# Performance work log

Hardware: AMD Instinct MI355X
Metric: run time of the kernel (lower is better)

The kernel has to match this reference:

```python
import jax, jax.numpy as jnp
import numpy as np

SIZE = 100
NUM_PARAMS = 5
DEPTH = 10            # complete binary tree: 2**DEPTH - 1 = 1023 nodes, 512 leaves
NUM_TREES = 1024
NUM_NODES = 2 ** DEPTH - 1


def setup_inputs() -> dict:
    key = jax.random.key(0)
    ks = jax.random.split(key, 7)
    times = jax.random.uniform(ks[0], (NUM_TREES, NUM_NODES), dtype=jnp.float32) + 0.1
    # Linear(1, size): weight column vector + bias
    Qw = jax.random.normal(ks[1], (SIZE,), dtype=jnp.float32) * 0.5
    Qb = jax.random.normal(ks[2], (SIZE,), dtype=jnp.float32) * 0.1
    # Linear(size, size): scaled so deep relu chain stays stable
    Ww = jax.random.normal(ks[3], (SIZE, SIZE), dtype=jnp.float32) * (0.5 / np.sqrt(SIZE))
    Wb = jax.random.normal(ks[4], (SIZE,), dtype=jnp.float32) * 0.1
    # Linear(size, num_params)
    Pw = jax.random.normal(ks[5], (NUM_PARAMS, SIZE), dtype=jnp.float32) * (1.0 / np.sqrt(SIZE))
    Pb = jax.random.normal(ks[6], (NUM_PARAMS,), dtype=jnp.float32) * 0.1
    return {"times": times, "Qw": Qw, "Qb": Qb, "Ww": Ww, "Wb": Wb, "Pw": Pw, "Pb": Pb}


def reference(times, Qw, Qb, Ww, Wb, Pw, Pb):
    """Batched, level-synchronous version of gRNN.traverse over complete binary trees.

    times: [B, 2**D - 1] node times in heap order (node i -> children 2i+1, 2i+2).
    Leaf:     h = relu(Q(t))
    Internal: h = relu(W(h_left + h_right) + Q(t))
    Root output projected to num_params. Same math as the recursive torch code.
    """
    B, N = times.shape
    D = int(np.log2(N + 1))
    # leaf level (deepest): Q(t) = t * Qw + Qb  (Linear(1, size))
    s = 2 ** (D - 1) - 1
    h = jax.nn.relu(times[:, s:s + 2 ** (D - 1), None] * Qw + Qb)  # [B, 2^(D-1), size]
    for d in range(D - 2, -1, -1):  # fixed small loop over tree depth
        s = 2 ** d - 1
        t = times[:, s:s + 2 ** d, None]                 # [B, 2^d, 1]
        comb = h[:, 0::2] + h[:, 1::2]                   # left + right children
        h = jax.nn.relu(jnp.einsum('bns,os->bno', comb, Ww) + Wb + t * Qw + Qb)
    root = h[:, 0]                                       # [B, size]
    return root @ Pw.T + Pb                              # [B, num_params]
```

## Files before the change

### kernel.cpp

```cpp
#include <hip/hip_runtime.h>

typedef _Float16 h8 __attribute__((ext_vector_type(8)));
typedef _Float16 h4 __attribute__((ext_vector_type(4)));
typedef float f4 __attribute__((ext_vector_type(4)));
typedef unsigned int uint32;

#define NT 7
#define KC 4
#define HSTRIDE 108

__global__ __launch_bounds__(256, 2)
void grnn_fused(const float* __restrict__ times,
                const float* __restrict__ Qw,
                const float* __restrict__ Qb,
                const float* __restrict__ Ww,
                const float* __restrict__ Wb,
                const float* __restrict__ Pw,
                const float* __restrict__ Pb,
                float* __restrict__ out)
{
  __shared__ __align__(16) _Float16 Hs[256][HSTRIDE];
  __shared__ __align__(8)  _Float16 ts[1026];
  __shared__ __align__(16) float qw_s[128];
  __shared__ __align__(16) float qb_s[128];

  const int tid  = threadIdx.x;
  const int wave = tid >> 6;
  const int lane = tid & 63;
  const int l15  = lane & 15;
  const int kg   = lane >> 4;
  const int tree = blockIdx.x;

  {
    const float* tg = times + tree * 1023;
    for (int i = tid; i < 1023; i += 256) ts[1 + i] = (_Float16)tg[i];
    if (tid == 0) ts[0] = (_Float16)0.f;
    if (tid < 128) {
      float qw = 0.f, qb = 0.f;
      if (tid < 100) { qw = Qw[tid]; qb = Qb[tid]; }
      qw_s[tid] = qw; qb_s[tid] = qb;
    }
  }

  h8 wf[NT][KC];
  #pragma unroll
  for (int nt = 0; nt < NT; ++nt) {
    const int r = nt * 16 + l15;
    #pragma unroll
    for (int kc = 0; kc < KC; ++kc) {
      h8 v;
      #pragma unroll
      for (int j = 0; j < 8; ++j) v[j] = (_Float16)0.f;
      if (r < 100) {
        const int kb = kc * 32 + kg * 8;
        if (kc < 3) {
          const f4 w0 = *(const f4*)&Ww[r * 100 + kb];
          const f4 w1 = *(const f4*)&Ww[r * 100 + kb + 4];
          #pragma unroll
          for (int j = 0; j < 4; ++j) {
            v[j]     = (_Float16)w0[j];
            v[j + 4] = (_Float16)w1[j];
          }
        } else if (kg == 0) {
          const f4 w0 = *(const f4*)&Ww[r * 100 + 96];
          #pragma unroll
          for (int j = 0; j < 4; ++j) v[j] = (_Float16)w0[j];
          v[4] = (_Float16)Qw[r];
          v[5] = (_Float16)(Qb[r] + Wb[r]);
        }
      }
      wf[nt][kc] = v;
    }
  }
  __syncthreads();

#define DO_MT(MT) do {                                                        \
    _Pragma("unroll")                                                         \
    for (int nt_ = 0; nt_ < NT; ++nt_) {                                      \
      f4 acc_ = {0.f, 0.f, 0.f, 0.f};                                         \
      _Pragma("unroll")                                                       \
      for (int kc_ = 0; kc_ < KC; ++kc_)                                      \
        acc_ = __builtin_amdgcn_mfma_f32_16x16x32_f16(af[kc_], wf[nt_][kc_],  \
                                                      acc_, 0, 0, 0);         \
      const int o_ = nt_ * 16 + l15;                                          \
      if (o_ < 100) {                                                         \
        const int mr_ = (MT) * 16 + kg * 4;                                   \
        _Pragma("unroll")                                                     \
        for (int r_ = 0; r_ < 4; ++r_)                                        \
          Hs[mr_ + r_][o_] = (_Float16)fmaxf(acc_[r_], 0.f);                  \
      }                                                                       \
    }                                                                         \
  } while (0)

#define LOAD_AFR(MT, S) do {                                                  \
    const int m2_ = ((MT) * 16 + l15) * 2;                                    \
    _Pragma("unroll")                                                         \
    for (int kc_ = 0; kc_ < 3; ++kc_) {                                       \
      const int kb_ = kc_ * 32 + kg * 8;                                      \
      h4 a0_ = *(const h4*)&Hs[m2_][kb_];                                     \
      h4 b0_ = *(const h4*)&Hs[m2_][kb_ + 4];                                 \
      h4 a1_ = *(const h4*)&Hs[m2_ + 1][kb_];                                 \
      h4 b1_ = *(const h4*)&Hs[m2_ + 1][kb_ + 4];                             \
      h4 lo_ = a0_ + a1_, hi_ = b0_ + b1_;                                    \
      af[kc_] = __builtin_shufflevector(lo_, hi_, 0, 1, 2, 3, 4, 5, 6, 7);    \
    }                                                                         \
    if (kg == 0) {                                                            \
      h4 a0_ = *(const h4*)&Hs[m2_][96];                                      \
      h4 a1_ = *(const h4*)&Hs[m2_ + 1][96];                                  \
      h4 lo_ = a0_ + a1_;                                                     \
      h4 hi_ = {ts[1 + (S) + (MT) * 16 + l15], (_Float16)1.f,                 \
                (_Float16)0.f, (_Float16)0.f};                                \
      af[3] = __builtin_shufflevector(lo_, hi_, 0, 1, 2, 3, 4, 5, 6, 7);      \
    } else {                                                                  \
      _Pragma("unroll")                                                       \
      for (int j_ = 0; j_ < 8; ++j_) af[3][j_] = (_Float16)0.f;               \
    }                                                                         \
  } while (0)

  #pragma unroll 1
  for (int i = 0; i < 4; ++i) {
    const int mt = wave + 4 * i;
    const int m  = mt * 16 + l15;
    const uint32 tp = *(const uint32*)&ts[512 + 2 * m];
    const float t0 = (float)*(const _Float16*)&tp;
    const float t1 = (float)*((const _Float16*)&tp + 1);
    h8 af[KC];
    #pragma unroll
    for (int kc = 0; kc < KC; ++kc) {
      const int kb = kc * 32 + kg * 8;
      const f4 qwa = *(const f4*)&qw_s[kb];
      const f4 qwb = *(const f4*)&qw_s[kb + 4];
      const f4 qba = *(const f4*)&qb_s[kb];
      const f4 qbb = *(const f4*)&qb_s[kb + 4];
      #pragma unroll
      for (int j = 0; j < 4; ++j) {
        float h0 = fmaxf(t0 * qwa[j] + qba[j], 0.f);
        float h1 = fmaxf(t1 * qwa[j] + qba[j], 0.f);
        af[kc][j] = (_Float16)(h0 + h1);
        float g0 = fmaxf(t0 * qwb[j] + qbb[j], 0.f);
        float g1 = fmaxf(t1 * qwb[j] + qbb[j], 0.f);
        af[kc][j + 4] = (_Float16)(g0 + g1);
      }
    }
    if (kg == 0) {
      af[3][4] = ts[1 + 255 + m];
      af[3][5] = (_Float16)1.f;
      af[3][6] = (_Float16)0.f;
      af[3][7] = (_Float16)0.f;
    }
    DO_MT(mt);
  }

  #pragma unroll 1
  for (int d = 7; d >= 0; --d) {
    const int s  = (1 << d) - 1;
    const int nm = (d >= 4) ? (1 << (d - 4)) : 1;
    const bool mine = wave < (nm < 4 ? nm : 4);
    h8 af[KC];
    if (mine) LOAD_AFR(wave, s);
    __syncthreads();
    if (mine) {
      DO_MT(wave);
      if (nm == 8) {
        LOAD_AFR(wave + 4, s);
        DO_MT(wave + 4);
      }
    }
    __syncthreads();
  }

  if (tid < 160) {
    const int p = tid >> 5;
    const int j = tid & 31;
    float sum = 0.f;
    #pragma unroll
    for (int c = 0; c < 4; ++c) {
      const int o = j + 32 * c;
      if (o < 100) sum += (float)Hs[0][o] * Pw[p * 100 + o];
    }
    sum += __shfl_down(sum, 16, 32);
    sum += __shfl_down(sum, 8, 32);
    sum += __shfl_down(sum, 4, 32);
    sum += __shfl_down(sum, 2, 32);
    sum += __shfl_down(sum, 1, 32);
    if (j == 0) out[tree * 5 + p] = sum + Pb[p];
  }
#undef DO_MT
#undef LOAD_AFR
}

extern "C" void kernel_launch(void* const* d_in, const int* in_sizes, int n_in,
                              void* d_out, int out_size, void* d_ws, size_t ws_size,
                              hipStream_t stream) {
  (void)n_in; (void)out_size; (void)d_ws; (void)ws_size;
  const float* times = (const float*)d_in[0];
  const float* Qw = (const float*)d_in[1];
  const float* Qb = (const float*)d_in[2];
  const float* Ww = (const float*)d_in[3];
  const float* Wb = (const float*)d_in[4];
  const float* Pw = (const float*)d_in[5];
  const float* Pb = (const float*)d_in[6];
  float* outp = (float*)d_out;
  const int B = in_sizes[0] / 1023;
  grnn_fused<<<dim3(B), dim3(256), 0, stream>>>(times, Qw, Qb, Ww, Wb, Pw, Pb, outp);
}
```

Measured before the change: 105.3 us.

## Pre-sum sibling children in registers, double-buffer LDS, and split upper levels across waves

The MFMA operands are swapped so each lane holds outputs of adjacent nodes. Sibling outputs are then summed with a lane shuffle before being written to LDS as combined child rows. LDS is double-buffered (read/write halves alternate per level), which drops one __syncthreads per level, and loads become single h8 reads with no adds. For the small upper levels the output tiles are split across all four waves instead of leaving three idle. This adds shuffles and more complex indexing, and risks correctness in the buffer indexing.

New measurement: 106.6 us. No clear change (+1.3%).

```diff
diff --git a/kernel.cpp b/kernel.cpp
--- a/kernel.cpp
+++ b/kernel.cpp
@@ -7,7 +7,7 @@
 
 #define NT 7
 #define KC 4
-#define HSTRIDE 108
+#define HSTRIDE 104
 
 __global__ __launch_bounds__(256, 2)
 void grnn_fused(const float* __restrict__ times,
@@ -19,7 +19,7 @@
                 const float* __restrict__ Pb,
                 float* __restrict__ out)
 {
-  __shared__ __align__(16) _Float16 Hs[256][HSTRIDE];
+  __shared__ __align__(16) _Float16 Cs[192][HSTRIDE];
   __shared__ __align__(8)  _Float16 ts[1026];
   __shared__ __align__(16) float qw_s[128];
   __shared__ __align__(16) float qb_s[128];
@@ -74,40 +74,58 @@
   }
   __syncthreads();
 
-#define DO_MT(MT) do {                                                        \
+#define DO_MT(MT, LO, HI, WB) do {                                            \
     _Pragma("unroll")                                                         \
     for (int nt_ = 0; nt_ < NT; ++nt_) {                                      \
-      f4 acc_ = {0.f, 0.f, 0.f, 0.f};                                         \
-      _Pragma("unroll")                                                       \
-      for (int kc_ = 0; kc_ < KC; ++kc_)                                      \
-        acc_ = __builtin_amdgcn_mfma_f32_16x16x32_f16(af[kc_], wf[nt_][kc_],  \
-                                                      acc_, 0, 0, 0);         \
-      const int o_ = nt_ * 16 + l15;                                          \
-      if (o_ < 100) {                                                         \
-        const int mr_ = (MT) * 16 + kg * 4;                                   \
+      if (nt_ >= (LO) && nt_ < (HI)) {                                        \
+        f4 acc_ = {0.f, 0.f, 0.f, 0.f};                                       \
         _Pragma("unroll")                                                     \
-        for (int r_ = 0; r_ < 4; ++r_)                                        \
-          Hs[mr_ + r_][o_] = (_Float16)fmaxf(acc_[r_], 0.f);                  \
+        for (int kc_ = 0; kc_ < KC; ++kc_)                                    \
+          acc_ = __builtin_amdgcn_mfma_f32_16x16x32_f16(wf[nt_][kc_],         \
+                                                        af[kc_], acc_, 0,0,0);\
+        if (nt_ < 6 || kg == 0) {                                             \
+          h4 hv_ = {(_Float16)fmaxf(acc_[0], 0.f),                            \
+                    (_Float16)fmaxf(acc_[1], 0.f),                            \
+                    (_Float16)fmaxf(acc_[2], 0.f),                            \
+                    (_Float16)fmaxf(acc_[3], 0.f)};                           \
+          uint2 u_ = __builtin_bit_cast(uint2, hv_);                          \
+          u_.x = __shfl_xor(u_.x, 1, 64);                                     \
+          u_.y = __shfl_xor(u_.y, 1, 64);                                     \
+          hv_ = hv_ + __builtin_bit_cast(h4, u_);                             \
+          if ((l15 & 1) == 0)                                                 \
+            *(h4*)&Cs[(WB) + (MT) * 8 + (l15 >> 1)][nt_ * 16 + kg * 4] = hv_; \
+        }                                                                     \
       }                                                                       \
     }                                                                         \
   } while (0)
 
-#define LOAD_AFR(MT, S) do {                                                  \
-    const int m2_ = ((MT) * 16 + l15) * 2;                                    \
+#define DO_MT_ROOT(LO, HI) do {                                               \
     _Pragma("unroll")                                                         \
-    for (int kc_ = 0; kc_ < 3; ++kc_) {                                       \
-      const int kb_ = kc_ * 32 + kg * 8;                                      \
-      h4 a0_ = *(const h4*)&Hs[m2_][kb_];                                     \
-      h4 b0_ = *(const h4*)&Hs[m2_][kb_ + 4];                                 \
-      h4 a1_ = *(const h4*)&Hs[m2_ + 1][kb_];                                 \
-      h4 b1_ = *(const h4*)&Hs[m2_ + 1][kb_ + 4];                             \
-      h4 lo_ = a0_ + a1_, hi_ = b0_ + b1_;                                    \
-      af[kc_] = __builtin_shufflevector(lo_, hi_, 0, 1, 2, 3, 4, 5, 6, 7);    \
+    for (int nt_ = 0; nt_ < NT; ++nt_) {                                      \
+      if (nt_ >= (LO) && nt_ < (HI)) {                                        \
+        f4 acc_ = {0.f, 0.f, 0.f, 0.f};                                       \
+        _Pragma("unroll")                                                     \
+        for (int kc_ = 0; kc_ < KC; ++kc_)                                    \
+          acc_ = __builtin_amdgcn_mfma_f32_16x16x32_f16(wf[nt_][kc_],         \
+                                                        af[kc_], acc_, 0,0,0);\
+        if ((nt_ < 6 || kg == 0) && l15 == 0) {                               \
+          h4 hv_ = {(_Float16)fmaxf(acc_[0], 0.f),                            \
+                    (_Float16)fmaxf(acc_[1], 0.f),                            \
+                    (_Float16)fmaxf(acc_[2], 0.f),                            \
+                    (_Float16)fmaxf(acc_[3], 0.f)};                           \
+          *(h4*)&Cs[0][nt_ * 16 + kg * 4] = hv_;                              \
+        }                                                                     \
+      }                                                                       \
     }                                                                         \
+  } while (0)
+
+#define LOAD_AFR(MT, S, RB) do {                                              \
+    const int row_ = (RB) + (MT) * 16 + l15;                                  \
+    _Pragma("unroll")                                                         \
+    for (int kc_ = 0; kc_ < 3; ++kc_)                                         \
+      af[kc_] = *(const h8*)&Cs[row_][kc_ * 32 + kg * 8];                     \
     if (kg == 0) {                                                            \
-      h4 a0_ = *(const h4*)&Hs[m2_][96];                                      \
-      h4 a1_ = *(const h4*)&Hs[m2_ + 1][96];                                  \
-      h4 lo_ = a0_ + a1_;                                                     \
+      h4 lo_ = *(const h4*)&Cs[row_][96];                                     \
       h4 hi_ = {ts[1 + (S) + (MT) * 16 + l15], (_Float16)1.f,                 \
                 (_Float16)0.f, (_Float16)0.f};                                \
       af[3] = __builtin_shufflevector(lo_, hi_, 0, 1, 2, 3, 4, 5, 6, 7);      \
@@ -148,26 +166,47 @@
       af[3][6] = (_Float16)0.f;
       af[3][7] = (_Float16)0.f;
     }
-    DO_MT(mt);
-  }
+    DO_MT(mt, 0, NT, 0);
+  }
+  __syncthreads();
 
   #pragma unroll 1
-  for (int d = 7; d >= 0; --d) {
+  for (int d = 7; d >= 1; --d) {
     const int s  = (1 << d) - 1;
+    const int R  = ((7 - d) & 1) ? 128 : 0;
+    const int W  = 128 - R;
     const int nm = (d >= 4) ? (1 << (d - 4)) : 1;
-    const bool mine = wave < (nm < 4 ? nm : 4);
     h8 af[KC];
-    if (mine) LOAD_AFR(wave, s);
+    if (nm >= 4) {
+      LOAD_AFR(wave, s, R);
+      DO_MT(wave, 0, NT, W);
+      if (nm == 8) {
+        LOAD_AFR(wave + 4, s, R);
+        DO_MT(wave + 4, 0, NT, W);
+      }
+    } else if (nm == 2) {
+      const int mt = wave & 1;
+      const int lo = (wave < 2) ? 0 : 4;
+      const int hi = (wave < 2) ? 4 : NT;
+      LOAD_AFR(mt, s, R);
+      DO_MT(mt, lo, hi, W);
+    } else {
+      const int lo = 2 * wave;
+      const int hi = (wave == 3) ? NT : 2 * wave + 2;
+      LOAD_AFR(0, s, R);
+      DO_MT(0, lo, hi, W);
+    }
     __syncthreads();
-    if (mine) {
-      DO_MT(wave);
-      if (nm == 8) {
-        LOAD_AFR(wave + 4, s);
-        DO_MT(wave + 4);
-      }
-    }
-    __syncthreads();
-  }
+  }
+
+  {
+    h8 af[KC];
+    const int lo = 2 * wave;
+    const int hi = (wave == 3) ? NT : 2 * wave + 2;
+    LOAD_AFR(0, 0, 128);
+    DO_MT_ROOT(lo, hi);
+  }
+  __syncthreads();
 
   if (tid < 160) {
     const int p = tid >> 5;
@@ -176,7 +215,7 @@
     #pragma unroll
     for (int c = 0; c < 4; ++c) {
       const int o = j + 32 * c;
-      if (o < 100) sum += (float)Hs[0][o] * Pw[p * 100 + o];
+      if (o < 100) sum += (float)Cs[0][o] * Pw[p * 100 + o];
     }
     sum += __shfl_down(sum, 16, 32);
     sum += __shfl_down(sum, 8, 32);
@@ -186,6 +225,7 @@
     if (j == 0) out[tree * 5 + p] = sum + Pb[p];
   }
 #undef DO_MT
+#undef DO_MT_ROOT
 #undef LOAD_AFR
 }
 
```
